# Kernel tuning notes

Hardware: AMD Instinct MI355X
Metric: run time of the kernel (lower is better)

## Reference

```python
import jax, jax.numpy as jnp
import numpy as np

V = 256   # input_size / vocab
H = 1024  # hidden_size
B = 32
S = 512


def _uniform_w(key, shape, fan_in):
    k = float(np.sqrt(1.0 / fan_in))
    return jax.random.uniform(key, shape, minval=-k, maxval=k, dtype=jnp.float32)


def setup_inputs() -> dict:
    key = jax.random.key(0)
    ks = jax.random.split(key, 8)
    x = jax.random.randint(ks[0], (B, S), 0, V)
    # Gate order along last dim: [i, f, g, o] (concatenated per-gate weights,
    # mathematically identical to 8 separate small matmuls in the original).
    W_x0 = jnp.concatenate([_uniform_w(k, (V, H), V) for k in jax.random.split(ks[1], 4)], axis=1)
    W_h0 = jnp.concatenate([_uniform_w(k, (H, H), H) for k in jax.random.split(ks[2], 4)], axis=1)
    W_x1 = jnp.concatenate([_uniform_w(k, (H, H), H) for k in jax.random.split(ks[3], 4)], axis=1)
    W_h1 = jnp.concatenate([_uniform_w(k, (H, H), H) for k in jax.random.split(ks[4], 4)], axis=1)
    # biases: b_i=0, b_f=1, b_g=0, b_o=0
    b_gate = jnp.concatenate([jnp.zeros(H), jnp.ones(H), jnp.zeros(H), jnp.zeros(H)])
    b0 = b_gate
    b1 = b_gate
    W_hy = _uniform_w(ks[5], (H, V), H)
    b_y = jnp.zeros((V,), dtype=jnp.float32)
    return {"x": x, "W_x0": W_x0, "W_h0": W_h0, "b0": b0,
            "W_x1": W_x1, "W_h1": W_h1, "b1": b1,
            "W_hy": W_hy, "b_y": b_y}


def _cell(gates, c_prev):
    i, f, g, o = jnp.split(gates, 4, axis=-1)
    c = jax.nn.sigmoid(f) * c_prev + jax.nn.sigmoid(i) * jnp.tanh(g)
    h = jax.nn.sigmoid(o) * jnp.tanh(c)
    return h, c


def reference(x, W_x0, W_h0, b0, W_x1, W_h1, b1, W_hy, b_y):
    # x: (B, S) int -> one-hot (S, B, V)
    xe = jax.nn.one_hot(x, V, dtype=W_x0.dtype)          # (B, S, V)
    # precompute layer-0 input projection for all timesteps (same math)
    xproj = jnp.einsum('bsv,vg->sbg', xe, W_x0) + b0     # (S, B, 4H)

    def step(carry, xp_t):
        h0, c0, h1, c1 = carry
        h0n, c0n = _cell(xp_t + h0 @ W_h0, c0)
        h1n, c1n = _cell(h0n @ W_x1 + h1 @ W_h1 + b1, c1)
        out = h1n @ W_hy + b_y                           # (B, V)
        return (h0n, c0n, h1n, c1n), out

    z = jnp.zeros((x.shape[0], H), dtype=W_x0.dtype)
    _, outs = jax.lax.scan(step, (z, z, z, z), xproj)
    return outs                                          # (S, B, V)
```

## Files before the change

kernel.cpp:

```cpp
#include <hip/hip_runtime.h>
#include <math.h>


typedef __attribute__((ext_vector_type(8))) short short8;
typedef __attribute__((ext_vector_type(4))) float f32x4;

constexpr int kV = 256, kH = 1024, kB = 32, kS = 512, G4H = 4096;
constexpr int NT = 512, NBLK = 208;
constexpr int NA = 64, B0 = 64, C0 = 192, ROOT = NBLK - 1;

constexpr long SZW = 4194304L;
constexpr long SZY = 262144L;
constexpr long WP0H = 0,        WP0L = SZW;
constexpr long WP1XH = 2*SZW,   WP1XL = 3*SZW;
constexpr long WP1HH = 4*SZW,   WP1HL = 5*SZW;
constexpr long WYH  = 6*SZW,    WYL  = 6*SZW + SZY;
constexpr long HOFF = 6*SZW + 2*SZY;
constexpr long RSLOT = 32768L;
constexpr long RING  = 513L;
constexpr long H0H = HOFF;
constexpr long H0L = HOFF + RING * RSLOT;
constexpr long H1H = HOFF + 2 * RING * RSLOT;
constexpr long H1L = HOFF + 3 * RING * RSLOT;
constexpr long FLG = HOFF + 4 * RING * RSLOT;

#define MFMA(a,b,c) __builtin_amdgcn_mfma_f32_16x16x32_bf16(a, b, c, 0, 0, 0)

#define VM_WAIT(n) do { \
    asm volatile("s_waitcnt vmcnt(" #n ")" ::: "memory"); \
    __builtin_amdgcn_sched_barrier(0); \
  } while (0)

#define WLOAD(dst, p) \
  asm volatile("global_load_dwordx4 %0, %1, off" : "=v"(dst) : "v"(p) : "memory")

__device__ __forceinline__ float sigmoidf_(float v) { return 1.f / (1.f + expf(-v)); }

__device__ __forceinline__ void bf16split(float w, unsigned& hi, unsigned& lo) {
  unsigned u = __float_as_uint(w);
  unsigned r = (u + 0x7fffu + ((u >> 16) & 1u)) >> 16;
  float res = w - __uint_as_float(r << 16);
  unsigned u2 = __float_as_uint(res);
  unsigned r2 = (u2 + 0x7fffu + ((u2 >> 16) & 1u)) >> 16;
  hi = r; lo = r2;
}


__device__ __forceinline__ void coh_store_u32(unsigned* p, unsigned v) {
  asm volatile("global_store_dword %0, %1, off sc0 sc1" :: "v"(p), "v"(v) : "memory");
}
__device__ __forceinline__ void coh_store_u16(unsigned short* p, unsigned v) {
  asm volatile("global_store_short %0, %1, off sc0 sc1" :: "v"(p), "v"(v) : "memory");
}
__device__ __forceinline__ unsigned coh_load_u32(const unsigned* p) {
  unsigned v;
  asm volatile("global_load_dword %0, %1, off sc0 sc1\n\ts_waitcnt vmcnt(0)"
               : "=v"(v) : "v"(p) : "memory");
  return v;
}

__device__ __forceinline__ void stage_issue4(const unsigned short* pr0h,
                                             const unsigned short* pr1h,
                                             const unsigned short* pr0l,
                                             const unsigned short* pr1l,
                                             int qoff,
                                             float4& a, float4& b,
                                             float4& c, float4& d) {
  asm volatile(
      "global_load_dwordx4 %0, %4, off\n\t"
      "global_load_dwordx4 %1, %5, off\n\t"
      "global_load_dwordx4 %2, %6, off\n\t"
      "global_load_dwordx4 %3, %7, off"
      : "=&v"(a), "=&v"(b), "=&v"(c), "=&v"(d)
      : "v"(pr0h + qoff), "v"(pr1h + qoff), "v"(pr0l + qoff), "v"(pr1l + qoff)
      : "memory");
}

__device__ __forceinline__ void stage_write4(short8* HH, short8* HL,
                                             int b0_, int kg,
                                             const float4& a, const float4& b,
                                             const float4& c, const float4& d) {
  HH[b0_ * 33 + kg]        = __builtin_bit_cast(short8, a);
  HH[(b0_ + 16) * 33 + kg] = __builtin_bit_cast(short8, b);
  HL[b0_ * 33 + kg]        = __builtin_bit_cast(short8, c);
  HL[(b0_ + 16) * 33 + kg] = __builtin_bit_cast(short8, d);
}

__device__ __forceinline__ void lds_barrier() {
  asm volatile("s_waitcnt lgkmcnt(0)" ::: "memory");
  __builtin_amdgcn_sched_barrier(0);
  __builtin_amdgcn_s_barrier();
  __builtin_amdgcn_sched_barrier(0);
}


__device__ __forceinline__ void flag_barrier(unsigned* arrive, unsigned* gen,
                                             int blk, int tid, int t) {
  __syncthreads();
  const unsigned target = (unsigned)(t + 1);
  if (tid == 0) coh_store_u32(arrive + blk * 16, target);
  if (blk == ROOT) {
    if (tid < 64) {
      const unsigned* q0 = arrive + tid * 16;
      const unsigned* q1 = arrive + (64 + tid) * 16;
      const unsigned* q2 = arrive + (128 + tid) * 16;
      const int i3 = (192 + tid < NBLK) ? (192 + tid) : 0;
      const unsigned* q3 = arrive + i3 * 16;
      int guard = 0;
      for (;;) {
        unsigned a, b, c, d;
        asm volatile(
            "global_load_dword %0, %4, off sc0 sc1\n\t"
            "global_load_dword %1, %5, off sc0 sc1\n\t"
            "global_load_dword %2, %6, off sc0 sc1\n\t"
            "global_load_dword %3, %7, off sc0 sc1\n\t"
            "s_waitcnt vmcnt(0)"
            : "=&v"(a), "=&v"(b), "=&v"(c), "=&v"(d)
            : "v"(q0), "v"(q1), "v"(q2), "v"(q3) : "memory");
        bool ok = (a >= target) && (b >= target) && (c >= target) && (d >= target);
        if (__all(ok)) break;
        if (++guard > (1 << 17)) break;
      }
      if (tid == 0) coh_store_u32(gen, target);
    }
  } else {
    if (tid == 0) {
      int guard = 0;
      while (coh_load_u32(gen) < target) {
        __builtin_amdgcn_s_sleep(1);
        if (++guard > (1 << 17)) break;
      }
    }
  }
  __syncthreads();
}


__global__ void pack_w(const float* __restrict__ in, unsigned short* __restrict__ hi,
                       unsigned short* __restrict__ lo, int ncols) {
  int id = blockIdx.x * 256 + threadIdx.x;
  int slab = id / ncols, row = id % ncols;
  int k0 = (slab >> 2) * 32 + (slab & 3) * 8;
  long ob = ((long)slab * ncols + row) * 8;
  #pragma unroll
  for (int e = 0; e < 8; ++e) {
    float w = in[(long)(k0 + e) * ncols + row];
    unsigned h_, l_;
    bf16split(w, h_, l_);
    hi[ob + e] = (unsigned short)h_;
    lo[ob + e] = (unsigned short)l_;
  }
}

__global__ void zero_init(unsigned short* __restrict__ wss) {
  long i = (long)blockIdx.x * 256 + threadIdx.x;
  if (i < 65536) {
    int arr = (int)(i >> 14), off = (int)(i & 16383);
    unsigned* p = (unsigned*)(wss + HOFF + (long)arr * (RING * RSLOT));
    coh_store_u32(p + off, 0u);
  } else if (i < 65536 + 4100) {
    unsigned* f = (unsigned*)(wss + FLG);
    coh_store_u32(f + (int)(i - 65536), 0u);
  }
}


extern "C" __global__ void __launch_bounds__(512, 1)
lstm_persist(const int* __restrict__ x,
             const float* __restrict__ Wx0,
             const float* __restrict__ b0v,
             const float* __restrict__ b1v,
             const float* __restrict__ byv,
             unsigned short* __restrict__ wss,
             float* __restrict__ out) {
  const short8* wp0h  = (const short8*)(wss + WP0H);
  const short8* wp0l  = (const short8*)(wss + WP0L);
  const short8* wp1xh = (const short8*)(wss + WP1XH);
  const short8* wp1xl = (const short8*)(wss + WP1XL);
  const short8* wp1hh = (const short8*)(wss + WP1HH);
  const short8* wp1hl = (const short8*)(wss + WP1HL);
  const short8* wyh   = (const short8*)(wss + WYH);
  const short8* wyl   = (const short8*)(wss + WYL);
  unsigned short* h0h = wss + H0H;
  unsigned short* h0l = wss + H0L;
  unsigned short* h1h = wss + H1H;
  unsigned short* h1l = wss + H1L;
  unsigned* arrive = (unsigned*)(wss + FLG);
  unsigned* gen = arrive + 4096;

  const int tid = threadIdx.x, blk = blockIdx.x;
  const int lane = tid & 63, m = lane & 15, quad = lane >> 4, w = tid >> 6;
  const int b0_ = tid >> 5, kg = tid & 31;
  const int kg8 = kg * 8;

  __shared__ short8 HSH[2][32 * 33];
  __shared__ short8 HSL[2][32 * 33];
  __shared__ float gx[4096];

  if (blk < NA) {
    const int g = w >> 1, kh = w & 1, j0A = blk * 16;
    const int ue = tid >> 5, be = tid & 31, j2e = j0A + ue;
    const float bA0 = b0v[j2e],          bA1 = b0v[kH + j2e];
    const float bA2 = b0v[2 * kH + j2e], bA3 = b0v[3 * kH + j2e];
    const short8* ah_ = wp0h + quad * 4096 + (g * 1024 + j0A + m);
    const short8* al_ = wp0l + quad * 4096 + (g * 1024 + j0A + m);
    short8 wah[16], wal[16];
    #pragma unroll
    for (int i = 0; i < 16; ++i) {
      WLOAD(wah[i], &ah_[(2 * i + kh) * 16384]);
      WLOAD(wal[i], &al_[(2 * i + kh) * 16384]);
    }
    VM_WAIT(0);
    float c0r = 0.f;

    #pragma unroll 1
    for (int t = 0; t < kS + 2; ++t) {
      const int s = t;
      if (s < kS) {
        const unsigned short* pH0 = h0h + (long)s * RSLOT + b0_ * 1024 + kg8;
        const unsigned short* pH1 = pH0 + 16 * 1024;
        const unsigned short* pL0 = h0l + (long)s * RSLOT + b0_ * 1024 + kg8;
        const unsigned short* pL1 = pL0 + 16 * 1024;
        const int xs = x[be * kS + s];
        const float* wxp = Wx0 + (long)xs * G4H + j2e;
        float wxi, wxf, wxg, wxo;
        asm volatile(
            "global_load_dword %0, %4, off\n\t"
            "global_load_dword %1, %5, off\n\t"
            "global_load_dword %2, %6, off\n\t"
            "global_load_dword %3, %7, off"
            : "=&v"(wxi), "=&v"(wxf), "=&v"(wxg), "=&v"(wxo)
            : "v"(wxp), "v"(wxp + kH), "v"(wxp + 2 * kH), "v"(wxp + 3 * kH)
            : "memory");
        float4 st[2][4];
        stage_issue4(pH0, pH1, pL0, pL1, 0, st[0][0], st[0][1], st[0][2], st[0][3]);
        f32x4 acc0 = {0.f, 0.f, 0.f, 0.f}, acc1 = {0.f, 0.f, 0.f, 0.f};
        #pragma unroll
        for (int ph = 0; ph < 4; ++ph) {
          if (ph < 3)
            stage_issue4(pH0, pH1, pL0, pL1, (ph + 1) * 256,
                         st[(ph + 1) & 1][0], st[(ph + 1) & 1][1],
                         st[(ph + 1) & 1][2], st[(ph + 1) & 1][3]);
          if (ph < 3) { VM_WAIT(4); } else { VM_WAIT(0); }
          stage_write4(&HSH[ph & 1][0], &HSL[ph & 1][0], b0_, kg,
                       st[ph & 1][0], st[ph & 1][1], st[ph & 1][2], st[ph & 1][3]);
          lds_barrier();
          #pragma unroll
          for (int i2 = 0; i2 < 4; ++i2) {
            const int kl = 2 * i2 + kh;
            const int widx = ph * 4 + i2;
            short8 bh0 = HSH[ph & 1][m * 33 + kl * 4 + quad];
            short8 bl0 = HSL[ph & 1][m * 33 + kl * 4 + quad];
            short8 bh1 = HSH[ph & 1][(16 + m) * 33 + kl * 4 + quad];
            short8 bl1 = HSL[ph & 1][(16 + m) * 33 + kl * 4 + quad];
            acc0 = MFMA(wah[widx], bh0, acc0);
            acc0 = MFMA(wah[widx], bl0, acc0);
            acc0 = MFMA(wal[widx], bh0, acc0);
            acc1 = MFMA(wah[widx], bh1, acc1);
            acc1 = MFMA(wah[widx], bl1, acc1);
            acc1 = MFMA(wal[widx], bh1, acc1);
          }
        }
        #pragma unroll
        for (int r = 0; r < 4; ++r) {
          gx[(kh * 64 + g * 16 + quad * 4 + r) * 32 + m]      = acc0[r];
          gx[(kh * 64 + g * 16 + quad * 4 + r) * 32 + 16 + m] = acc1[r];
        }
        lds_barrier();
        {
          float gi = gx[(0 + ue) * 32 + be]  + gx[(64 + 0 + ue) * 32 + be]  + wxi + bA0;
          float gf = gx[(16 + ue) * 32 + be] + gx[(64 + 16 + ue) * 32 + be] + wxf + bA1;
          float gg = gx[(32 + ue) * 32 + be] + gx[(64 + 32 + ue) * 32 + be] + wxg + bA2;
          float go = gx[(48 + ue) * 32 + be] + gx[(64 + 48 + ue) * 32 + be] + wxo + bA3;
          float cc = sigmoidf_(gf) * c0r + sigmoidf_(gi) * tanhf(gg);
          float hh = sigmoidf_(go) * tanhf(cc);
          c0r = cc;
          unsigned h_, l_;
          bf16split(hh, h_, l_);
          coh_store_u16(h0h + (long)(s + 1) * RSLOT + be * 1024 + j2e, h_);
          coh_store_u16(h0l + (long)(s + 1) * RSLOT + be * 1024 + j2e, l_);
        }
      }
      if (t < kS + 1) flag_barrier(arrive, gen, blk, tid, t);
    }
  } else if (blk < C0) {
    const int hf = w >> 2, mt = (w >> 1) & 1, kq = w & 1;
    const int rowB = mt * 16 + m;
    const int growB = (rowB >> 3) * 1024 + (blk - B0) * 8 + (rowB & 7);
    const int ub = tid >> 5;
    const int j2b = (blk - B0) * 8 + (ub & 7);
    const float bB0 = b1v[j2b],          bB1 = b1v[kH + j2b];
    const float bB2 = b1v[2 * kH + j2b], bB3 = b1v[3 * kH + j2b];
    const short8* bh_ = (hf ? wp1hh : wp1xh) + quad * 4096 + growB;
    const short8* bl_ = (hf ? wp1hl : wp1xl) + quad * 4096 + growB;
    short8 wbh[16], wbl[16];
    #pragma unroll
    for (int i = 0; i < 16; ++i) {
      WLOAD(wbh[i], &bh_[(2 * i + kq) * 16384]);
      WLOAD(wbl[i], &bl_[(2 * i + kq) * 16384]);
    }
    VM_WAIT(0);
    float c1r = 0.f;

    #pragma unroll 1
    for (int t = 0; t < kS + 2; ++t) {
      const int s = t - 1;
      if (s >= 0 && s < kS) {
        const unsigned short* pA0h = h0h + (long)(s + 1) * RSLOT + b0_ * 1024 + kg8;
        const unsigned short* pA1h = pA0h + 16 * 1024;
        const unsigned short* pA0l = h0l + (long)(s + 1) * RSLOT + b0_ * 1024 + kg8;
        const unsigned short* pA1l = pA0l + 16 * 1024;
        const unsigned short* pB0h = h1h + (long)s * RSLOT + b0_ * 1024 + kg8;
        const unsigned short* pB1h = pB0h + 16 * 1024;
        const unsigned short* pB0l = h1l + (long)s * RSLOT + b0_ * 1024 + kg8;
        const unsigned short* pB1l = pB0l + 16 * 1024;
        float4 st[2][4];
        stage_issue4(pA0h, pA1h, pA0l, pA1l, 0,
                     st[0][0], st[0][1], st[0][2], st[0][3]);
        f32x4 acc0 = {0.f, 0.f, 0.f, 0.f}, acc1 = {0.f, 0.f, 0.f, 0.f};
        #pragma unroll
        for (int ph = 0; ph < 8; ++ph) {
          const int half = ph >> 2, qtr = ph & 3;
          if (ph < 7) {
            const int p1 = ph + 1, q1 = p1 & 3;
            if ((p1 >> 2) == 0)
              stage_issue4(pA0h, pA1h, pA0l, pA1l, q1 * 256,
                           st[p1 & 1][0], st[p1 & 1][1], st[p1 & 1][2], st[p1 & 1][3]);
            else
              stage_issue4(pB0h, pB1h, pB0l, pB1l, q1 * 256,
                           st[p1 & 1][0], st[p1 & 1][1], st[p1 & 1][2], st[p1 & 1][3]);
          }
          if (ph < 7) { VM_WAIT(4); } else { VM_WAIT(0); }
          stage_write4(&HSH[ph & 1][0], &HSL[ph & 1][0], b0_, kg,
                       st[ph & 1][0], st[ph & 1][1], st[ph & 1][2], st[ph & 1][3]);
          lds_barrier();
          if (hf == half) {
            #pragma unroll
            for (int i2 = 0; i2 < 4; ++i2) {
              const int kl = 2 * i2 + kq;
              const int widx = qtr * 4 + i2;
              short8 bh0 = HSH[ph & 1][m * 33 + kl * 4 + quad];
              short8 bl0 = HSL[ph & 1][m * 33 + kl * 4 + quad];
              short8 bh1 = HSH[ph & 1][(16 + m) * 33 + kl * 4 + quad];
              short8 bl1 = HSL[ph & 1][(16 + m) * 33 + kl * 4 + quad];
              acc0 = MFMA(wbh[widx], bh0, acc0);
              acc0 = MFMA(wbh[widx], bl0, acc0);
              acc0 = MFMA(wbl[widx], bh0, acc0);
              acc1 = MFMA(wbh[widx], bh1, acc1);
              acc1 = MFMA(wbh[widx], bl1, acc1);
              acc1 = MFMA(wbl[widx], bh1, acc1);
            }
          }
        }
        #pragma unroll
        for (int r = 0; r < 4; ++r) {
          const int rg = hf * 2 + kq;
          gx[(rg * 32 + mt * 16 + quad * 4 + r) * 32 + m]      = acc0[r];
          gx[(rg * 32 + mt * 16 + quad * 4 + r) * 32 + 16 + m] = acc1[r];
        }
        lds_barrier();
        if (tid < 256) {
          const int u = tid >> 5, b = tid & 31;
          float gt[4];
          #pragma unroll
          for (int g2 = 0; g2 < 4; ++g2) {
            const int row = g2 * 8 + u;
            gt[g2] = gx[(row) * 32 + b] + gx[(32 + row) * 32 + b] +
                     gx[(64 + row) * 32 + b] + gx[(96 + row) * 32 + b];
          }
          float gt0 = gt[0] + bB0, gt1 = gt[1] + bB1;
          float gt2 = gt[2] + bB2, gt3 = gt[3] + bB3;
          float cc = sigmoidf_(gt1) * c1r + sigmoidf_(gt0) * tanhf(gt2);
          float hh = sigmoidf_(gt3) * tanhf(cc);
          c1r = cc;
          unsigned h_, l_;
          bf16split(hh, h_, l_);
          const int j2 = (blk - B0) * 8 + u;
          coh_store_u16(h1h + (long)(s + 1) * RSLOT + b * 1024 + j2, h_);
          coh_store_u16(h1l + (long)(s + 1) * RSLOT + b * 1024 + j2, l_);
        }
      }
      if (t < kS + 1) flag_barrier(arrive, gen, blk, tid, t);
    }
  } else {
    const int growC = (blk - C0) * 16 + m;
    const float byr = byv[(blk - C0) * 16 + (tid & 15)];
    const short8* ch_ = wyh + quad * 256 + growC;
    const short8* cl_ = wyl + quad * 256 + growC;
    short8 wch[4], wcl[4];
    #pragma unroll
    for (int i = 0; i < 4; ++i) {
      WLOAD(wch[i], &ch_[(i * 8 + w) * 1024]);
      WLOAD(wcl[i], &cl_[(i * 8 + w) * 1024]);
    }
    VM_WAIT(0);

    #pragma unroll 1
    for (int t = 0; t < kS + 2; ++t) {
      const int s = t - 2;
      if (s >= 0 && s < kS) {
        const unsigned short* pH0 = h1h + (long)(s + 1) * RSLOT + b0_ * 1024 + kg8;
        const unsigned short* pH1 = pH0 + 16 * 1024;
        const unsigned short* pL0 = h1l + (long)(s + 1) * RSLOT + b0_ * 1024 + kg8;
        const unsigned short* pL1 = pL0 + 16 * 1024;
        float4 st[2][4];
        stage_issue4(pH0, pH1, pL0, pL1, 0, st[0][0], st[0][1], st[0][2], st[0][3]);
        f32x4 acc0 = {0.f, 0.f, 0.f, 0.f}, acc1 = {0.f, 0.f, 0.f, 0.f};
        #pragma unroll
        for (int ph = 0; ph < 4; ++ph) {
          if (ph < 3)
            stage_issue4(pH0, pH1, pL0, pL1, (ph + 1) * 256,
                         st[(ph + 1) & 1][0], st[(ph + 1) & 1][1],
                         st[(ph + 1) & 1][2], st[(ph + 1) & 1][3]);
          if (ph < 3) { VM_WAIT(4); } else { VM_WAIT(0); }
          stage_write4(&HSH[ph & 1][0], &HSL[ph & 1][0], b0_, kg,
                       st[ph & 1][0], st[ph & 1][1], st[ph & 1][2], st[ph & 1][3]);
          lds_barrier();
          {
            const int kl = w;
            short8 bh0 = HSH[ph & 1][m * 33 + kl * 4 + quad];
            short8 bl0 = HSL[ph & 1][m * 33 + kl * 4 + quad];
            short8 bh1 = HSH[ph & 1][(16 + m) * 33 + kl * 4 + quad];
            short8 bl1 = HSL[ph & 1][(16 + m) * 33 + kl * 4 + quad];
            acc0 = MFMA(wch[ph], bh0, acc0);
            acc0 = MFMA(wch[ph], bl0, acc0);
            acc0 = MFMA(wcl[ph], bh0, acc0);
            acc1 = MFMA(wch[ph], bh1, acc1);
            acc1 = MFMA(wch[ph], bl1, acc1);
            acc1 = MFMA(wcl[ph], bh1, acc1);
          }
        }
        #pragma unroll
        for (int r = 0; r < 4; ++r) {
          gx[(w * 16 + quad * 4 + r) * 32 + m]      = acc0[r];
          gx[(w * 16 + quad * 4 + r) * 32 + 16 + m] = acc1[r];
        }
        lds_barrier();
        {
          const int b = tid >> 4, vl = tid & 15;
          const int vg = (blk - C0) * 16 + vl;
          float sum = byr;
          #pragma unroll
          for (int rg = 0; rg < 8; ++rg) sum += gx[(rg * 16 + vl) * 32 + b];
          out[(s * kB + b) * kV + vg] = sum;
        }
      }
      if (t < kS + 1) flag_barrier(arrive, gen, blk, tid, t);
    }
  }
}


extern "C" void kernel_launch(void* const* d_in, const int* in_sizes, int n_in,
                              void* d_out, int out_size, void* d_ws, size_t ws_size,
                              hipStream_t stream) {
  const int*   x   = (const int*)d_in[0];
  const float* Wx0 = (const float*)d_in[1];
  const float* Wh0 = (const float*)d_in[2];
  const float* b0v = (const float*)d_in[3];
  const float* Wx1 = (const float*)d_in[4];
  const float* Wh1 = (const float*)d_in[5];
  const float* b1v = (const float*)d_in[6];
  const float* Why = (const float*)d_in[7];
  const float* byv = (const float*)d_in[8];
  unsigned short* wss = (unsigned short*)d_ws;
  float* outp = (float*)d_out;

  hipLaunchKernelGGL(pack_w, dim3(2048), dim3(256), 0, stream,
                     Wh0, wss + WP0H, wss + WP0L, G4H);
  hipLaunchKernelGGL(pack_w, dim3(2048), dim3(256), 0, stream,
                     Wx1, wss + WP1XH, wss + WP1XL, G4H);
  hipLaunchKernelGGL(pack_w, dim3(2048), dim3(256), 0, stream,
                     Wh1, wss + WP1HH, wss + WP1HL, G4H);
  hipLaunchKernelGGL(pack_w, dim3(128), dim3(256), 0, stream,
                     Why, wss + WYH, wss + WYL, kV);
  hipLaunchKernelGGL(zero_init, dim3(274), dim3(256), 0, stream, wss);

  hipLaunchKernelGGL(lstm_persist, dim3(NBLK), dim3(NT), 0, stream,
                     x, Wx0, b0v, b1v, byv, wss, outp);
}
```

Measured before the change: 4.363 ms.

## Split global grid barrier into hierarchical per-stage barriers and stage both layer-1 inputs together

Replaces the single root-collected grid barrier with a chained scheme. Layer-0 blocks sync among themselves and publish genA. Layer-1 blocks wait on their own arrivals plus genA and publish genB. Output blocks only wait on genB and no longer post arrival flags. Separately, layer-1 blocks now stage both the h0 and h1 inputs in one 4-phase loop using 8 LDS buffers, instead of 8 phases where half the waves sat idle. This cuts the number of LDS barriers and raises MFMA utilisation, at the cost of more LDS and more loads in flight. A risk is that output blocks no longer signal arrival, so producers could overwrite ring slots before consumers finish, although the 513-slot ring makes that unlikely.

After: 4.205 ms. 1.04x faster.

```diff
diff --git a/kernel.cpp b/kernel.cpp
--- a/kernel.cpp
+++ b/kernel.cpp
@@ -7,7 +7,7 @@
 
 constexpr int kV = 256, kH = 1024, kB = 32, kS = 512, G4H = 4096;
 constexpr int NT = 512, NBLK = 208;
-constexpr int NA = 64, B0 = 64, C0 = 192, ROOT = NBLK - 1;
+constexpr int NA = 64, B0 = 64, C0 = 192;
 
 constexpr long SZW = 4194304L;
 constexpr long SZY = 262144L;
@@ -94,42 +94,81 @@
 }
 
 
-__device__ __forceinline__ void flag_barrier(unsigned* arrive, unsigned* gen,
-                                             int blk, int tid, int t) {
+__device__ __forceinline__ void barrier_A(unsigned* arrive, unsigned* genA,
+                                          int blk, int tid, int t) {
   __syncthreads();
   const unsigned target = (unsigned)(t + 1);
   if (tid == 0) coh_store_u32(arrive + blk * 16, target);
-  if (blk == ROOT) {
+  if (blk == NA - 1) {
     if (tid < 64) {
       const unsigned* q0 = arrive + tid * 16;
-      const unsigned* q1 = arrive + (64 + tid) * 16;
-      const unsigned* q2 = arrive + (128 + tid) * 16;
-      const int i3 = (192 + tid < NBLK) ? (192 + tid) : 0;
-      const unsigned* q3 = arrive + i3 * 16;
       int guard = 0;
       for (;;) {
-        unsigned a, b, c, d;
-        asm volatile(
-            "global_load_dword %0, %4, off sc0 sc1\n\t"
-            "global_load_dword %1, %5, off sc0 sc1\n\t"
-            "global_load_dword %2, %6, off sc0 sc1\n\t"
-            "global_load_dword %3, %7, off sc0 sc1\n\t"
-            "s_waitcnt vmcnt(0)"
-            : "=&v"(a), "=&v"(b), "=&v"(c), "=&v"(d)
-            : "v"(q0), "v"(q1), "v"(q2), "v"(q3) : "memory");
-        bool ok = (a >= target) && (b >= target) && (c >= target) && (d >= target);
-        if (__all(ok)) break;
+        unsigned a;
+        asm volatile("global_load_dword %0, %1, off sc0 sc1\n\ts_waitcnt vmcnt(0)"
+                     : "=&v"(a) : "v"(q0) : "memory");
+        if (__all(a >= target)) break;
         if (++guard > (1 << 17)) break;
       }
-      if (tid == 0) coh_store_u32(gen, target);
+      if (tid == 0) coh_store_u32(genA, target);
     }
   } else {
     if (tid == 0) {
       int guard = 0;
-      while (coh_load_u32(gen) < target) {
+      while (coh_load_u32(genA) < target) {
         __builtin_amdgcn_s_sleep(1);
         if (++guard > (1 << 17)) break;
       }
+    }
+  }
+  __syncthreads();
+}
+
+__device__ __forceinline__ void barrier_B(unsigned* arrive, unsigned* genA,
+                                          unsigned* genB, int blk, int tid, int t) {
+  __syncthreads();
+  const unsigned target = (unsigned)(t + 1);
+  if (tid == 0) coh_store_u32(arrive + blk * 16, target);
+  if (blk == C0 - 1) {
+    if (tid < 64) {
+      const unsigned* q1 = arrive + (64 + tid) * 16;
+      const unsigned* q2 = arrive + (128 + tid) * 16;
+      int guard = 0;
+      for (;;) {
+        unsigned b, c, ga;
+        asm volatile(
+            "global_load_dword %0, %3, off sc0 sc1\n\t"
+            "global_load_dword %1, %4, off sc0 sc1\n\t"
+            "global_load_dword %2, %5, off sc0 sc1\n\t"
+            "s_waitcnt vmcnt(0)"
+            : "=&v"(b), "=&v"(c), "=&v"(ga)
+            : "v"(q1), "v"(q2), "v"(genA) : "memory");
+        bool ok = (b >= target) && (c >= target) && (ga >= target);
+        if (__all(ok)) break;
+        if (++guard > (1 << 17)) break;
+      }
+      if (tid == 0) coh_store_u32(genB, target);
+    }
+  } else {
+    if (tid == 0) {
+      int guard = 0;
+      while (coh_load_u32(genB) < target) {
+        __builtin_amdgcn_s_sleep(1);
+        if (++guard > (1 << 17)) break;
+      }
+    }
+  }
+  __syncthreads();
+}
+
+__device__ __forceinline__ void barrier_C(unsigned* genB, int tid, int t) {
+  __syncthreads();
+  const unsigned target = (unsigned)(t + 1);
+  if (tid == 0) {
+    int guard = 0;
+    while (coh_load_u32(genB) < target) {
+      __builtin_amdgcn_s_sleep(1);
+      if (++guard > (1 << 17)) break;
     }
   }
   __syncthreads();
@@ -158,7 +197,7 @@
     int arr = (int)(i >> 14), off = (int)(i & 16383);
     unsigned* p = (unsigned*)(wss + HOFF + (long)arr * (RING * RSLOT));
     coh_store_u32(p + off, 0u);
-  } else if (i < 65536 + 4100) {
+  } else if (i < 65536 + 4160) {
     unsigned* f = (unsigned*)(wss + FLG);
     coh_store_u32(f + (int)(i - 65536), 0u);
   }
@@ -186,15 +225,15 @@
   unsigned short* h1h = wss + H1H;
   unsigned short* h1l = wss + H1L;
   unsigned* arrive = (unsigned*)(wss + FLG);
-  unsigned* gen = arrive + 4096;
+  unsigned* genA = arrive + 4096;
+  unsigned* genB = arrive + 4112;
 
   const int tid = threadIdx.x, blk = blockIdx.x;
   const int lane = tid & 63, m = lane & 15, quad = lane >> 4, w = tid >> 6;
   const int b0_ = tid >> 5, kg = tid & 31;
   const int kg8 = kg * 8;
 
-  __shared__ short8 HSH[2][32 * 33];
-  __shared__ short8 HSL[2][32 * 33];
+  __shared__ short8 LB[8][32 * 33];
   __shared__ float gx[4096];
 
   if (blk < NA) {
@@ -242,17 +281,17 @@
                          st[(ph + 1) & 1][0], st[(ph + 1) & 1][1],
                          st[(ph + 1) & 1][2], st[(ph + 1) & 1][3]);
           if (ph < 3) { VM_WAIT(4); } else { VM_WAIT(0); }
-          stage_write4(&HSH[ph & 1][0], &HSL[ph & 1][0], b0_, kg,
+          stage_write4(&LB[ph & 1][0], &LB[2 + (ph & 1)][0], b0_, kg,
                        st[ph & 1][0], st[ph & 1][1], st[ph & 1][2], st[ph & 1][3]);
           lds_barrier();
           #pragma unroll
           for (int i2 = 0; i2 < 4; ++i2) {
             const int kl = 2 * i2 + kh;
             const int widx = ph * 4 + i2;
-            short8 bh0 = HSH[ph & 1][m * 33 + kl * 4 + quad];
-            short8 bl0 = HSL[ph & 1][m * 33 + kl * 4 + quad];
-            short8 bh1 = HSH[ph & 1][(16 + m) * 33 + kl * 4 + quad];
-            short8 bl1 = HSL[ph & 1][(16 + m) * 33 + kl * 4 + quad];
+            short8 bh0 = LB[ph & 1][m * 33 + kl * 4 + quad];
+            short8 bl0 = LB[2 + (ph & 1)][m * 33 + kl * 4 + quad];
+            short8 bh1 = LB[ph & 1][(16 + m) * 33 + kl * 4 + quad];
+            short8 bl1 = LB[2 + (ph & 1)][(16 + m) * 33 + kl * 4 + quad];
             acc0 = MFMA(wah[widx], bh0, acc0);
             acc0 = MFMA(wah[widx], bl0, acc0);
             acc0 = MFMA(wal[widx], bh0, acc0);
@@ -281,7 +320,7 @@
           coh_store_u16(h0l + (long)(s + 1) * RSLOT + be * 1024 + j2e, l_);
         }
       }
-      if (t < kS + 1) flag_barrier(arrive, gen, blk, tid, t);
+      if (t < kS + 1) barrier_A(arrive, genA, blk, tid, t);
     }
   } else if (blk < C0) {
     const int hf = w >> 2, mt = (w >> 1) & 1, kq = w & 1;
@@ -314,42 +353,44 @@
         const unsigned short* pB1h = pB0h + 16 * 1024;
         const unsigned short* pB0l = h1l + (long)s * RSLOT + b0_ * 1024 + kg8;
         const unsigned short* pB1l = pB0l + 16 * 1024;
-        float4 st[2][4];
+        float4 sa[2][4], sb[2][4];
         stage_issue4(pA0h, pA1h, pA0l, pA1l, 0,
-                     st[0][0], st[0][1], st[0][2], st[0][3]);
+                     sa[0][0], sa[0][1], sa[0][2], sa[0][3]);
+        stage_issue4(pB0h, pB1h, pB0l, pB1l, 0,
+                     sb[0][0], sb[0][1], sb[0][2], sb[0][3]);
         f32x4 acc0 = {0.f, 0.f, 0.f, 0.f}, acc1 = {0.f, 0.f, 0.f, 0.f};
         #pragma unroll
-        for (int ph = 0; ph < 8; ++ph) {
-          const int half = ph >> 2, qtr = ph & 3;
-          if (ph < 7) {
-            const int p1 = ph + 1, q1 = p1 & 3;
-            if ((p1 >> 2) == 0)
-              stage_issue4(pA0h, pA1h, pA0l, pA1l, q1 * 256,
-                           st[p1 & 1][0], st[p1 & 1][1], st[p1 & 1][2], st[p1 & 1][3]);
-            else
-              stage_issue4(pB0h, pB1h, pB0l, pB1l, q1 * 256,
-                           st[p1 & 1][0], st[p1 & 1][1], st[p1 & 1][2], st[p1 & 1][3]);
+        for (int q = 0; q < 4; ++q) {
+          if (q < 3) {
+            stage_issue4(pA0h, pA1h, pA0l, pA1l, (q + 1) * 256,
+                         sa[(q + 1) & 1][0], sa[(q + 1) & 1][1],
+                         sa[(q + 1) & 1][2], sa[(q + 1) & 1][3]);
+            stage_issue4(pB0h, pB1h, pB0l, pB1l, (q + 1) * 256,
+                         sb[(q + 1) & 1][0], sb[(q + 1) & 1][1],
+                         sb[(q + 1) & 1][2], sb[(q + 1) & 1][3]);
           }
-          if (ph < 7) { VM_WAIT(4); } else { VM_WAIT(0); }
-          stage_write4(&HSH[ph & 1][0], &HSL[ph & 1][0], b0_, kg,
-                       st[ph & 1][0], st[ph & 1][1], st[ph & 1][2], st[ph & 1][3]);
+          if (q < 3) { VM_WAIT(8); } else { VM_WAIT(0); }
+          stage_write4(&LB[q & 1][0], &LB[2 + (q & 1)][0], b0_, kg,
+                       sa[q & 1][0], sa[q & 1][1], sa[q & 1][2], sa[q & 1][3]);
+          stage_write4(&LB[4 + (q & 1)][0], &LB[6 + (q & 1)][0], b0_, kg,
+                       sb[q & 1][0], sb[q & 1][1], sb[q & 1][2], sb[q & 1][3]);
           lds_barrier();
-          if (hf == half) {
-            #pragma unroll
-            for (int i2 = 0; i2 < 4; ++i2) {
-              const int kl = 2 * i2 + kq;
-              const int widx = qtr * 4 + i2;
-              short8 bh0 = HSH[ph & 1][m * 33 + kl * 4 + quad];
-              short8 bl0 = HSL[ph & 1][m * 33 + kl * 4 + quad];
-              short8 bh1 = HSH[ph & 1][(16 + m) * 33 + kl * 4 + quad];
-              short8 bl1 = HSL[ph & 1][(16 + m) * 33 + kl * 4 + quad];
-              acc0 = MFMA(wbh[widx], bh0, acc0);
-              acc0 = MFMA(wbh[widx], bl0, acc0);
-              acc0 = MFMA(wbl[widx], bh0, acc0);
-              acc1 = MFMA(wbh[widx], bh1, acc1);
-              acc1 = MFMA(wbh[widx], bl1, acc1);
-              acc1 = MFMA(wbl[widx], bh1, acc1);
-            }
+          const short8* GH = &LB[hf * 4 + (q & 1)][0];
+          const short8* GL = &LB[hf * 4 + 2 + (q & 1)][0];
+          #pragma unroll
+          for (int i2 = 0; i2 < 4; ++i2) {
+            const int kl = 2 * i2 + kq;
+            const int widx = q * 4 + i2;
+            short8 bh0 = GH[m * 33 + kl * 4 + quad];
+            short8 bl0 = GL[m * 33 + kl * 4 + quad];
+            short8 bh1 = GH[(16 + m) * 33 + kl * 4 + quad];
+            short8 bl1 = GL[(16 + m) * 33 + kl * 4 + quad];
+            acc0 = MFMA(wbh[widx], bh0, acc0);
+            acc0 = MFMA(wbh[widx], bl0, acc0);
+            acc0 = MFMA(wbl[widx], bh0, acc0);
+            acc1 = MFMA(wbh[widx], bh1, acc1);
+            acc1 = MFMA(wbh[widx], bl1, acc1);
+            acc1 = MFMA(wbl[widx], bh1, acc1);
           }
         }
         #pragma unroll
@@ -380,7 +421,7 @@
           coh_store_u16(h1l + (long)(s + 1) * RSLOT + b * 1024 + j2, l_);
         }
       }
-      if (t < kS + 1) flag_barrier(arrive, gen, blk, tid, t);
+      if (t < kS + 1) barrier_B(arrive, genA, genB, blk, tid, t);
     }
   } else {
     const int growC = (blk - C0) * 16 + m;
@@ -413,15 +454,15 @@
                          st[(ph + 1) & 1][0], st[(ph + 1) & 1][1],
                          st[(ph + 1) & 1][2], st[(ph + 1) & 1][3]);
           if (ph < 3) { VM_WAIT(4); } else { VM_WAIT(0); }
-          stage_write4(&HSH[ph & 1][0], &HSL[ph & 1][0], b0_, kg,
+          stage_write4(&LB[ph & 1][0], &LB[2 + (ph & 1)][0], b0_, kg,
                        st[ph & 1][0], st[ph & 1][1], st[ph & 1][2], st[ph & 1][3]);
           lds_barrier();
           {
             const int kl = w;
-            short8 bh0 = HSH[ph & 1][m * 33 + kl * 4 + quad];
-            short8 bl0 = HSL[ph & 1][m * 33 + kl * 4 + quad];
-            short8 bh1 = HSH[ph & 1][(16 + m) * 33 + kl * 4 + quad];
-            short8 bl1 = HSL[ph & 1][(16 + m) * 33 + kl * 4 + quad];
+            short8 bh0 = LB[ph & 1][m * 33 + kl * 4 + quad];
+            short8 bl0 = LB[2 + (ph & 1)][m * 33 + kl * 4 + quad];
+            short8 bh1 = LB[ph & 1][(16 + m) * 33 + kl * 4 + quad];
+            short8 bl1 = LB[2 + (ph & 1)][(16 + m) * 33 + kl * 4 + quad];
             acc0 = MFMA(wch[ph], bh0, acc0);
             acc0 = MFMA(wch[ph], bl0, acc0);
             acc0 = MFMA(wcl[ph], bh0, acc0);
@@ -445,7 +486,7 @@
           out[(s * kB + b) * kV + vg] = sum;
         }
       }
-      if (t < kS + 1) flag_barrier(arrive, gen, blk, tid, t);
+      if (t < kS + 1) barrier_C(genB, tid, t);
     }
   }
 }
```
